# Kernel tuning notes

Measured on AMD Instinct MI355X. Metric: run time of the kernel, lower is better.

The kernel has to match this reference:

```python
import jax, jax.numpy as jnp
import numpy as np

N_NODES = 100000
N_EDGES = 1600000
IN_DIM, HIDDEN_DIM, OUT_DIM = 500, 64, 40


def setup_inputs() -> dict:
    key = jax.random.key(0)
    k1, k2, k3, k4, k5 = jax.random.split(key, 5)
    x = jax.random.normal(k1, (N_NODES, IN_DIM), dtype=jnp.float32)
    edge_index = jax.random.randint(k2, (2, N_EDGES), 0, N_NODES, dtype=jnp.int64)
    # Glorot-style init like PyG GCNConv
    W1 = jax.random.normal(k3, (IN_DIM, HIDDEN_DIM), dtype=jnp.float32) / np.sqrt(IN_DIM)
    b1 = jnp.zeros((HIDDEN_DIM,), dtype=jnp.float32)
    W2 = jax.random.normal(k4, (HIDDEN_DIM, OUT_DIM), dtype=jnp.float32) / np.sqrt(HIDDEN_DIM)
    b2 = jnp.zeros((OUT_DIM,), dtype=jnp.float32)
    return {"x": x, "W1": W1, "b1": b1, "W2": W2, "b2": b2, "edge_index": edge_index}


def _gcn_conv(x, W, b, src, dst, n):
    """PyG GCNConv: h = D^{-1/2} (A + I) D^{-1/2} (x W) + b."""
    h = x @ W  # transform first, propagate in smaller dim
    loops = jnp.arange(n, dtype=src.dtype)
    s = jnp.concatenate([src, loops])
    d = jnp.concatenate([dst, loops])
    deg = jax.ops.segment_sum(jnp.ones_like(d, dtype=h.dtype), d, num_segments=n)
    dinv = jnp.where(deg > 0, jax.lax.rsqrt(deg), 0.0)
    norm = dinv[s] * dinv[d]               # [E+N]
    msg = h[s] * norm[:, None]             # gather + scale
    out = jax.ops.segment_sum(msg, d, num_segments=n)  # scatter-add
    return out + b


def reference(x, W1, b1, W2, b2, edge_index):
    src, dst = edge_index[0], edge_index[1]
    n = x.shape[0]
    h = _gcn_conv(x, W1, b1, src, dst, n)
    h = jax.nn.relu(h)  # eval mode: dropout is identity
    out = _gcn_conv(h, W2, b2, src, dst, n)
    return out
```

## Files before the change

kernel.cpp:

```cpp
#include <hip/hip_runtime.h>
#include <cstdint>
#include <cstddef>

#define NN 100000
#define NE 1600000
#define IND 500
#define HD 64
#define OD 40
#define NBLK ((NN + 255) / 256)
#define KSTEPS 16
#define NTT 16
#define EB 1563

typedef __attribute__((ext_vector_type(8))) short short8v;
typedef __attribute__((ext_vector_type(8))) __bf16 bf16x8;
typedef __attribute__((ext_vector_type(4))) float float4v;

template <class V>
static __device__ __forceinline__ auto mfma_bf16_(V a, V b, float4v c, int)
    -> decltype(__builtin_amdgcn_mfma_f32_16x16x32_bf16(a, b, c, 0, 0, 0)) {
    return __builtin_amdgcn_mfma_f32_16x16x32_bf16(a, b, c, 0, 0, 0);
}
template <class V>
static __device__ __forceinline__ float4v mfma_bf16_(V a, V b, float4v c, long) {
    return __builtin_amdgcn_mfma_f32_16x16x32_bf16((bf16x8)a, (bf16x8)b, c, 0, 0, 0);
}
static __device__ __forceinline__ float4v mfma16(short8v a, short8v b, float4v c) {
    return mfma_bf16_(a, b, c, 0);
}

static __device__ __forceinline__ float bf2f(unsigned short v) {
    return __uint_as_float((unsigned)v << 16);
}
static __device__ __forceinline__ unsigned short f2bf(float v) {
    unsigned u = __float_as_uint(v);
    return (unsigned short)((u + 0x7fffu + ((u >> 16) & 1u)) >> 16);
}

typedef __attribute__((address_space(3))) char lds_char;
typedef const __attribute__((address_space(1))) char g_char;
static __device__ __forceinline__ void gl16(const char* g, char* l) {
    __builtin_amdgcn_global_load_lds((g_char*)g, (lds_char*)l, 16, 0, 0);
}

static __device__ __forceinline__ int detect64(const void* ei) {
    const unsigned* u = (const unsigned*)ei;
    int is64 = 1;
    #pragma unroll
    for (int i = 1; i < 16; i += 2)
        if (u[i] != 0u) is64 = 0;
    return is64;
}

static __device__ __forceinline__ void load4e(const void* ei, int is64, size_t base, int v[4]) {
    if (is64) {
        int4 a = ((const int4*)ei)[base >> 1];
        int4 b = ((const int4*)ei)[(base >> 1) + 1];
        v[0] = a.x; v[1] = a.z; v[2] = b.x; v[3] = b.z;
    } else {
        int4 a = *(const int4*)((const int*)ei + base);
        v[0] = a.x; v[1] = a.y; v[2] = a.z; v[3] = a.w;
    }
}

__global__ __launch_bounds__(256) void k_count_prep(const void* ei, int* cnt,
                                                    int* __restrict__ rank,
                                                    const float* __restrict__ W,
                                                    unsigned short* __restrict__ wh,
                                                    unsigned short* __restrict__ wl) {
    const int is64 = detect64(ei);
    int e0 = (blockIdx.x * 256 + threadIdx.x) * 4;
    if (e0 < NE) {
        int d[4];
        load4e(ei, is64, (size_t)NE + e0, d);
        int4 r;
        r.x = atomicAdd(&cnt[d[0]], 1);
        r.y = atomicAdd(&cnt[d[1]], 1);
        r.z = atomicAdd(&cnt[d[2]], 1);
        r.w = atomicAdd(&cnt[d[3]], 1);
        *(int4*)(rank + e0) = r;
    }
    int t = blockIdx.x * 256 + threadIdx.x;
    if (t < KSTEPS * 4 * 64) {
        int l = t & 63;
        int f = (t >> 6) & 3;
        int s = t >> 8;
        int n = f * 16 + (l & 15);
        int kbase = s * 32 + 8 * (l >> 4);
        unsigned short* ph = wh + (size_t)t * 8;
        unsigned short* pl = wl + (size_t)t * 8;
        #pragma unroll
        for (int j = 0; j < 8; ++j) {
            int k = kbase + j;
            float v = (k < IND) ? W[(size_t)k * HD + n] : 0.f;
            unsigned u = __float_as_uint(v);
            ph[j] = (unsigned short)(u >> 16);
            float r = v - __uint_as_float(u & 0xffff0000u);
            pl[j] = f2bf(r);
        }
    }
}

__global__ __launch_bounds__(256) void k_scan_block(const int* __restrict__ cnt,
                                                    int* __restrict__ rowptr,
                                                    int* __restrict__ bsum,
                                                    float* __restrict__ dinv) {
    int t = threadIdx.x;
    int i = blockIdx.x * 256 + t;
    int v = (i < NN) ? cnt[i] : 0;
    if (i < NN) dinv[i] = rsqrtf((float)v + 1.0f);
    int inc = v;
    #pragma unroll
    for (int off = 1; off < 64; off <<= 1) {
        int u = __shfl_up(inc, off);
        if ((t & 63) >= off) inc += u;
    }
    __shared__ int wsum[4];
    if ((t & 63) == 63) wsum[t >> 6] = inc;
    __syncthreads();
    if (t == 0) {
        int a = 0;
        #pragma unroll
        for (int w = 0; w < 4; ++w) { int b = wsum[w]; wsum[w] = a; a += b; }
        bsum[blockIdx.x] = a;
    }
    __syncthreads();
    if (i < NN) rowptr[i] = inc - v + wsum[t >> 6];
}

__global__ __launch_bounds__(512) void k_scan_bsum(int* bsum) {
    int t = threadIdx.x;
    int v = (t < NBLK) ? bsum[t] : 0;
    int inc = v;
    #pragma unroll
    for (int off = 1; off < 64; off <<= 1) {
        int u = __shfl_up(inc, off);
        if ((t & 63) >= off) inc += u;
    }
    __shared__ int wsum[8];
    if ((t & 63) == 63) wsum[t >> 6] = inc;
    __syncthreads();
    if (t == 0) {
        int a = 0;
        #pragma unroll
        for (int w = 0; w < 8; ++w) { int b = wsum[w]; wsum[w] = a; a += b; }
    }
    __syncthreads();
    if (t < NBLK) bsum[t] = inc - v + wsum[t >> 6];
}

__global__ void k_scan_add(int* rowptr, const int* __restrict__ bsum) {
    int i = blockIdx.x * 256 + threadIdx.x;
    if (i < NN) rowptr[i] += bsum[i >> 8];
    if (i == 0) rowptr[NN] = NE;
}

static __device__ __forceinline__ void split8f(float4 u0, float4 u1,
                                               short8v& hi, short8v& lo) {
    float t[8] = {u0.x, u0.y, u0.z, u0.w, u1.x, u1.y, u1.z, u1.w};
    #pragma unroll
    for (int j = 0; j < 8; ++j) {
        unsigned q = __float_as_uint(t[j]);
        hi[j] = (short)(q >> 16);
        float r = t[j] - __uint_as_float(q & 0xffff0000u);
        lo[j] = (short)f2bf(r);
    }
}

__global__ __launch_bounds__(256, 5) void k_gemm1m(const float* __restrict__ x,
                                                   const char* __restrict__ whb,
                                                   const char* __restrict__ wlb,
                                                   const float* __restrict__ dinv,
                                                   unsigned short* __restrict__ h,
                                                   const void* __restrict__ ei,
                                                   const int* __restrict__ rowptr,
                                                   const int* __restrict__ rank,
                                                   int* __restrict__ srcs) {
    __shared__ char smem[32768];
    const int tid  = threadIdx.x;
    const int lane = tid & 63;
    const int wave = tid >> 6;
    const int row0 = blockIdx.x * 64;
    const int rA = lane & 15;
    const int cg = lane >> 4;

    auto stage = [&](int kt, int buf) {
        const bool tail = (kt == NTT - 1);
        #pragma unroll
        for (int i = 0; i < 2; ++i) {
            int slot = i * 256 + tid;
            int r = slot >> 3, c = slot & 7;
            int cs = c ^ (r & 7);
            if (tail && cs > 4) cs = 4;
            int rsrc = row0 + r; if (rsrc >= NN) rsrc = NN - 1;
            const char* g = (const char*)x + (size_t)rsrc * (IND * 4) + kt * 128 + cs * 16;
            char* l = smem + buf * 16384 + (i * 256 + wave * 64) * 16;
            gl16(g, l);
        }
        #pragma unroll
        for (int i = 0; i < 2; ++i) {
            int j = i * 256 + tid;
            const char* src = (j < 256 ? whb : wlb) + kt * 4096 + (size_t)(j & 255) * 16;
            char* l = smem + buf * 16384 + 8192 + (i * 256 + wave * 64) * 16;
            gl16(src, l);
        }
    };

    float4v acc[4];
    const float4v zero4 = {0.f, 0.f, 0.f, 0.f};
    #pragma unroll
    for (int f = 0; f < 4; ++f) acc[f] = zero4;

    stage(0, 0);
    stage(1, 1);

    const int rbase = (wave * 16 + rA) * 8;
    const int sw = rA & 7;

    for (int kt = 0; kt < NTT; ++kt) {
        if (kt + 1 < NTT) asm volatile("s_waitcnt vmcnt(4)\ns_barrier" ::: "memory");
        else              asm volatile("s_waitcnt vmcnt(0)\ns_barrier" ::: "memory");
        const float4*  pa = (const float4*)(smem + (kt & 1) * 16384);
        const short8v* pb = (const short8v*)(smem + (kt & 1) * 16384 + 8192);
        int ch = cg * 2;
        float4 u0 = pa[rbase + (ch ^ sw)];
        float4 u1 = pa[rbase + ((ch + 1) ^ sw)];
        short8v ah, al;
        split8f(u0, u1, ah, al);
        #pragma unroll
        for (int f = 0; f < 4; ++f) {
            short8v vh = pb[f * 64 + lane];
            short8v vl = pb[256 + f * 64 + lane];
            acc[f] = mfma16(al, vh, acc[f]);
            acc[f] = mfma16(ah, vl, acc[f]);
            acc[f] = mfma16(ah, vh, acc[f]);
        }
        if (kt + 2 < NTT) {
            asm volatile("s_barrier" ::: "memory");
            stage(kt + 2, kt & 1);
        }
    }

    #pragma unroll
    for (int j = 0; j < 4; ++j) {
        int row = row0 + wave * 16 + cg * 4 + j;
        if (row < NN) {
            float dv = dinv[row];
            #pragma unroll
            for (int f = 0; f < 4; ++f)
                h[(size_t)row * HD + f * 16 + rA] = f2bf(acc[f][j] * dv);
        }
    }

    {
        int e0 = (blockIdx.x * 256 + tid) * 4;
        if (e0 < NE) {
            const int is64 = detect64(ei);
            int s[4], d[4];
            load4e(ei, is64, (size_t)e0, s);
            load4e(ei, is64, (size_t)NE + e0, d);
            int4 r = *(const int4*)(rank + e0);
            srcs[rowptr[d[0]] + r.x] = s[0];
            srcs[rowptr[d[1]] + r.y] = s[1];
            srcs[rowptr[d[2]] + r.z] = s[2];
            srcs[rowptr[d[3]] + r.w] = s[3];
        }
    }
}

static __device__ __forceinline__ float csr_gather(const int* __restrict__ rowptr,
                                                   const int* __restrict__ srcs,
                                                   const unsigned short* __restrict__ hb,
                                                   int wid, int lane, float acc) {
    int beg = rowptr[wid];
    int cnt = rowptr[wid + 1] - beg;
    for (int base = 0; base < cnt; base += 64) {
        int m = cnt - base; if (m > 64) m = 64;
        int sj = (lane < m) ? srcs[beg + base + lane] : 0;
        int j = 0;
        for (; j + 16 <= m; j += 16) {
            float v[16];
            #pragma unroll
            for (int q = 0; q < 16; ++q) {
                int sq = __builtin_amdgcn_readlane(sj, j + q);
                v[q] = bf2f(hb[(size_t)sq * HD + lane]);
            }
            float t0 = ((v[0] + v[1]) + (v[2] + v[3])) + ((v[4] + v[5]) + (v[6] + v[7]));
            float t1 = ((v[8] + v[9]) + (v[10] + v[11])) + ((v[12] + v[13]) + (v[14] + v[15]));
            acc += t0 + t1;
        }
        if (j + 8 <= m) {
            float v[8];
            #pragma unroll
            for (int q = 0; q < 8; ++q) {
                int sq = __builtin_amdgcn_readlane(sj, j + q);
                v[q] = bf2f(hb[(size_t)sq * HD + lane]);
            }
            acc += ((v[0] + v[1]) + (v[2] + v[3])) + ((v[4] + v[5]) + (v[6] + v[7]));
            j += 8;
        }
        for (; j < m; ++j) {
            int s = __builtin_amdgcn_readlane(sj, j);
            acc += bf2f(hb[(size_t)s * HD + lane]);
        }
    }
    return acc;
}

__global__ __launch_bounds__(256) void k_agg1(const int* __restrict__ rowptr,
                                              const int* __restrict__ srcs,
                                              const float* __restrict__ dinv,
                                              const unsigned short* __restrict__ hb,
                                              const float* __restrict__ bias,
                                              unsigned short* __restrict__ outb) {
    int wid = (blockIdx.x * 256 + threadIdx.x) >> 6;
    int lane = threadIdx.x & 63;
    if (wid >= NN) return;
    float acc = bf2f(hb[(size_t)wid * HD + lane]);
    acc = csr_gather(rowptr, srcs, hb, wid, lane, acc);
    float dn = dinv[wid];
    outb[(size_t)wid * HD + lane] = f2bf(fmaxf(acc * dn + bias[lane], 0.f) * dn);
}

__global__ __launch_bounds__(256) void k_agg2_gemm2(const int* __restrict__ rowptr,
                                                    const int* __restrict__ srcs,
                                                    const float* __restrict__ dinv,
                                                    const unsigned short* __restrict__ hb,
                                                    const float* __restrict__ W2,
                                                    const float* __restrict__ b2,
                                                    float* __restrict__ out) {
    __shared__ float ws2[HD][OD];
    __shared__ float hsh[4][HD];
    const int t = threadIdx.x;
    for (int i = t; i < HD * OD; i += 256)
        ws2[i / OD][i % OD] = W2[i];

    int wid = (blockIdx.x * 256 + t) >> 6;
    int lane = t & 63;
    int w = t >> 6;
    float acc = bf2f(hb[(size_t)wid * HD + lane]);
    acc = csr_gather(rowptr, srcs, hb, wid, lane, acc);
    hsh[w][lane] = acc * dinv[wid];
    __syncthreads();
    if (lane < OD) {
        float s = b2[lane];
        #pragma unroll
        for (int k = 0; k < HD; ++k)
            s = fmaf(hsh[w][k], ws2[k][lane], s);
        out[(size_t)wid * OD + lane] = s;
    }
}

extern "C" void kernel_launch(void* const* d_in, const int* in_sizes, int n_in,
                              void* d_out, int out_size, void* d_ws, size_t ws_size,
                              hipStream_t stream) {
    const float* x  = (const float*)d_in[0];
    const float* W1 = (const float*)d_in[1];
    const float* b1 = (const float*)d_in[2];
    const float* W2 = (const float*)d_in[3];
    const float* b2 = (const float*)d_in[4];
    const void*  ei = d_in[5];
    float* out = (float*)d_out;

    char* ws = (char*)d_ws;
    unsigned short* h1b    = (unsigned short*)ws;
    unsigned short* hrelub = (unsigned short*)(ws + 12800000);
    int*   rowptr = (int*)(ws + 25600000);
    int*   cnt    = (int*)(ws + 26000896);
    int*   bsum   = (int*)(ws + 26401792);
    int*   srcs   = (int*)(ws + 26403840);
    int*   rank   = (int*)(ws + 32803840);
    float* dinv   = (float*)(ws + 39203840);
    unsigned short* wh = (unsigned short*)(ws + 39604224);
    unsigned short* wl = (unsigned short*)(ws + 39669760);

    hipMemsetAsync(cnt, 0, (size_t)NN * 4, stream);
    k_count_prep<<<EB, 256, 0, stream>>>(ei, cnt, rank, W1, wh, wl);
    k_scan_block<<<NBLK, 256, 0, stream>>>(cnt, rowptr, bsum, dinv);
    k_scan_bsum<<<1, 512, 0, stream>>>(bsum);
    k_scan_add<<<NBLK, 256, 0, stream>>>(rowptr, bsum);
    k_gemm1m<<<EB, 256, 0, stream>>>(x, (const char*)wh, (const char*)wl, dinv, h1b,
                                     ei, rowptr, rank, srcs);
    k_agg1<<<(NN * 64) / 256, 256, 0, stream>>>(rowptr, srcs, dinv, h1b, b1, hrelub);
    k_agg2_gemm2<<<(NN * 64) / 256, 256, 0, stream>>>(rowptr, srcs, dinv, hrelub, W2, b2, out);
}
```

Baseline: 307.9 us.

## Enlarge GEMM1 tile to 128 rows and split CSR scatter into its own kernel

The first-layer GEMM now processes 128 rows per block, two 64-row M-subtiles, and reuses the loaded W1 hi/lo fragments across both subtiles. This halves the weight staging per row and the block count. The CSR source scatter, previously fused into the GEMM epilogue, moves to a separate kernel, and the memset is replaced by a zeroing kernel. The costs are higher LDS and register use (occupancy bound lowered from 5 to 3) and two extra kernel launches.

```diff
diff --git a/kernel.cpp b/kernel.cpp
--- a/kernel.cpp
+++ b/kernel.cpp
@@ -11,6 +11,7 @@
 #define KSTEPS 16
 #define NTT 16
 #define EB 1563
+#define GB 782
 
 typedef __attribute__((ext_vector_type(8))) short short8v;
 typedef __attribute__((ext_vector_type(8))) __bf16 bf16x8;
@@ -61,6 +62,11 @@
         int4 a = *(const int4*)((const int*)ei + base);
         v[0] = a.x; v[1] = a.y; v[2] = a.z; v[3] = a.w;
     }
+}
+
+__global__ void k_zero(int* __restrict__ cnt) {
+    int i = blockIdx.x * 256 + threadIdx.x;
+    if (i < NN) cnt[i] = 0;
 }
 
 __global__ __launch_bounds__(256) void k_count_prep(const void* ei, int* cnt,
@@ -155,6 +161,21 @@
     if (i == 0) rowptr[NN] = NE;
 }
 
+__global__ void k_scatter(const void* ei, const int* __restrict__ rowptr,
+                          const int* __restrict__ rank, int* __restrict__ srcs) {
+    int e0 = (blockIdx.x * 256 + threadIdx.x) * 4;
+    if (e0 >= NE) return;
+    const int is64 = detect64(ei);
+    int s[4], d[4];
+    load4e(ei, is64, (size_t)e0, s);
+    load4e(ei, is64, (size_t)NE + e0, d);
+    int4 r = *(const int4*)(rank + e0);
+    srcs[rowptr[d[0]] + r.x] = s[0];
+    srcs[rowptr[d[1]] + r.y] = s[1];
+    srcs[rowptr[d[2]] + r.z] = s[2];
+    srcs[rowptr[d[3]] + r.w] = s[3];
+}
+
 static __device__ __forceinline__ void split8f(float4 u0, float4 u1,
                                                short8v& hi, short8v& lo) {
     float t[8] = {u0.x, u0.y, u0.z, u0.w, u1.x, u1.y, u1.z, u1.w};
@@ -167,73 +188,78 @@
     }
 }
 
-__global__ __launch_bounds__(256, 5) void k_gemm1m(const float* __restrict__ x,
+__global__ __launch_bounds__(256, 3) void k_gemm1m(const float* __restrict__ x,
                                                    const char* __restrict__ whb,
                                                    const char* __restrict__ wlb,
                                                    const float* __restrict__ dinv,
-                                                   unsigned short* __restrict__ h,
-                                                   const void* __restrict__ ei,
-                                                   const int* __restrict__ rowptr,
-                                                   const int* __restrict__ rank,
-                                                   int* __restrict__ srcs) {
-    __shared__ char smem[32768];
+                                                   unsigned short* __restrict__ h) {
+    __shared__ char smem[49152];
     const int tid  = threadIdx.x;
     const int lane = tid & 63;
     const int wave = tid >> 6;
-    const int row0 = blockIdx.x * 64;
+    const int row0 = blockIdx.x * 128;
     const int rA = lane & 15;
     const int cg = lane >> 4;
 
     auto stage = [&](int kt, int buf) {
         const bool tail = (kt == NTT - 1);
         #pragma unroll
-        for (int i = 0; i < 2; ++i) {
+        for (int i = 0; i < 4; ++i) {
             int slot = i * 256 + tid;
             int r = slot >> 3, c = slot & 7;
             int cs = c ^ (r & 7);
             if (tail && cs > 4) cs = 4;
             int rsrc = row0 + r; if (rsrc >= NN) rsrc = NN - 1;
             const char* g = (const char*)x + (size_t)rsrc * (IND * 4) + kt * 128 + cs * 16;
-            char* l = smem + buf * 16384 + (i * 256 + wave * 64) * 16;
+            char* l = smem + buf * 24576 + (i * 256 + wave * 64) * 16;
             gl16(g, l);
         }
         #pragma unroll
         for (int i = 0; i < 2; ++i) {
             int j = i * 256 + tid;
             const char* src = (j < 256 ? whb : wlb) + kt * 4096 + (size_t)(j & 255) * 16;
-            char* l = smem + buf * 16384 + 8192 + (i * 256 + wave * 64) * 16;
+            char* l = smem + buf * 24576 + 16384 + (i * 256 + wave * 64) * 16;
             gl16(src, l);
         }
     };
 
-    float4v acc[4];
+    float4v acc[2][4];
     const float4v zero4 = {0.f, 0.f, 0.f, 0.f};
     #pragma unroll
-    for (int f = 0; f < 4; ++f) acc[f] = zero4;
+    for (int mi = 0; mi < 2; ++mi)
+        #pragma unroll
+        for (int f = 0; f < 4; ++f) acc[mi][f] = zero4;
 
     stage(0, 0);
     stage(1, 1);
 
-    const int rbase = (wave * 16 + rA) * 8;
     const int sw = rA & 7;
+    const int ch = cg * 2;
 
     for (int kt = 0; kt < NTT; ++kt) {
-        if (kt + 1 < NTT) asm volatile("s_waitcnt vmcnt(4)\ns_barrier" ::: "memory");
+        if (kt + 1 < NTT) asm volatile("s_waitcnt vmcnt(6)\ns_barrier" ::: "memory");
         else              asm volatile("s_waitcnt vmcnt(0)\ns_barrier" ::: "memory");
-        const float4*  pa = (const float4*)(smem + (kt & 1) * 16384);
-        const short8v* pb = (const short8v*)(smem + (kt & 1) * 16384 + 8192);
-        int ch = cg * 2;
-        float4 u0 = pa[rbase + (ch ^ sw)];
-        float4 u1 = pa[rbase + ((ch + 1) ^ sw)];
-        short8v ah, al;
-        split8f(u0, u1, ah, al);
+        const float4*  pa = (const float4*)(smem + (kt & 1) * 24576);
+        const short8v* pb = (const short8v*)(smem + (kt & 1) * 24576 + 16384);
+        short8v vh[4], vl[4];
         #pragma unroll
         for (int f = 0; f < 4; ++f) {
-            short8v vh = pb[f * 64 + lane];
-            short8v vl = pb[256 + f * 64 + lane];
-            acc[f] = mfma16(al, vh, acc[f]);
-            acc[f] = mfma16(ah, vl, acc[f]);
-            acc[f] = mfma16(ah, vh, acc[f]);
+            vh[f] = pb[f * 64 + lane];
+            vl[f] = pb[256 + f * 64 + lane];
+        }
+        #pragma unroll
+        for (int mi = 0; mi < 2; ++mi) {
+            int rb = (mi * 64 + wave * 16 + rA) * 8;
+            float4 u0 = pa[rb + (ch ^ sw)];
+            float4 u1 = pa[rb + ((ch + 1) ^ sw)];
+            short8v ah, al;
+            split8f(u0, u1, ah, al);
+            #pragma unroll
+            for (int f = 0; f < 4; ++f) {
+                acc[mi][f] = mfma16(al, vh[f], acc[mi][f]);
+                acc[mi][f] = mfma16(ah, vl[f], acc[mi][f]);
+                acc[mi][f] = mfma16(ah, vh[f], acc[mi][f]);
+            }
         }
         if (kt + 2 < NTT) {
             asm volatile("s_barrier" ::: "memory");
@@ -242,30 +268,17 @@
     }
 
     #pragma unroll
-    for (int j = 0; j < 4; ++j) {
-        int row = row0 + wave * 16 + cg * 4 + j;
-        if (row < NN) {
-            float dv = dinv[row];
-            #pragma unroll
-            for (int f = 0; f < 4; ++f)
-                h[(size_t)row * HD + f * 16 + rA] = f2bf(acc[f][j] * dv);
-        }
-    }
-
-    {
-        int e0 = (blockIdx.x * 256 + tid) * 4;
-        if (e0 < NE) {
-            const int is64 = detect64(ei);
-            int s[4], d[4];
-            load4e(ei, is64, (size_t)e0, s);
-            load4e(ei, is64, (size_t)NE + e0, d);
-            int4 r = *(const int4*)(rank + e0);
-            srcs[rowptr[d[0]] + r.x] = s[0];
-            srcs[rowptr[d[1]] + r.y] = s[1];
-            srcs[rowptr[d[2]] + r.z] = s[2];
-            srcs[rowptr[d[3]] + r.w] = s[3];
-        }
-    }
+    for (int mi = 0; mi < 2; ++mi)
+        #pragma unroll
+        for (int j = 0; j < 4; ++j) {
+            int row = row0 + mi * 64 + wave * 16 + cg * 4 + j;
+            if (row < NN) {
+                float dv = dinv[row];
+                #pragma unroll
+                for (int f = 0; f < 4; ++f)
+                    h[(size_t)row * HD + f * 16 + rA] = f2bf(acc[mi][f][j] * dv);
+            }
+        }
 }
 
 static __device__ __forceinline__ float csr_gather(const int* __restrict__ rowptr,
@@ -374,13 +387,13 @@
     unsigned short* wh = (unsigned short*)(ws + 39604224);
     unsigned short* wl = (unsigned short*)(ws + 39669760);
 
-    hipMemsetAsync(cnt, 0, (size_t)NN * 4, stream);
+    k_zero<<<NBLK, 256, 0, stream>>>(cnt);
     k_count_prep<<<EB, 256, 0, stream>>>(ei, cnt, rank, W1, wh, wl);
     k_scan_block<<<NBLK, 256, 0, stream>>>(cnt, rowptr, bsum, dinv);
     k_scan_bsum<<<1, 512, 0, stream>>>(bsum);
     k_scan_add<<<NBLK, 256, 0, stream>>>(rowptr, bsum);
-    k_gemm1m<<<EB, 256, 0, stream>>>(x, (const char*)wh, (const char*)wl, dinv, h1b,
-                                     ei, rowptr, rank, srcs);
+    k_scatter<<<EB, 256, 0, stream>>>(ei, rowptr, rank, srcs);
+    k_gemm1m<<<GB, 256, 0, stream>>>(x, (const char*)wh, (const char*)wl, dinv, h1b);
     k_agg1<<<(NN * 64) / 256, 256, 0, stream>>>(rowptr, srcs, dinv, h1b, b1, hrelub);
     k_agg2_gemm2<<<(NN * 64) / 256, 256, 0, stream>>>(rowptr, srcs, dinv, hrelub, W2, b2, out);
 }
```

New measurement: 320.8 us. 4.2% more time.

## Vectorize CSR gather to 4 edges per wave and split scatter kernel

Applied to the files above, without the earlier changes.

The CSR aggregation now has each wave handle four neighbour rows at once. Each group of 16 lanes loads 8 bytes (four bf16 features) per neighbour instead of one 2-byte element per lane, and partial sums are folded across lane groups with xor shuffles. The aim is wider, fewer memory transactions for the random-row gathers in both aggregation kernels. Separately, the edge-to-CSR scatter moves out of the GEMM kernel into its own launch, which adds a kernel launch but removes the scatter tail from the GEMM blocks. Sums are now accumulated in a different order, so results may differ slightly in rounding.

```diff
diff --git a/kernel.cpp b/kernel.cpp
--- a/kernel.cpp
+++ b/kernel.cpp
@@ -155,6 +155,21 @@
     if (i == 0) rowptr[NN] = NE;
 }
 
+__global__ void k_scatter(const void* ei, const int* __restrict__ rowptr,
+                          const int* __restrict__ rank, int* __restrict__ srcs) {
+    int e0 = (blockIdx.x * 256 + threadIdx.x) * 4;
+    if (e0 >= NE) return;
+    const int is64 = detect64(ei);
+    int s[4], d[4];
+    load4e(ei, is64, (size_t)e0, s);
+    load4e(ei, is64, (size_t)NE + e0, d);
+    int4 r = *(const int4*)(rank + e0);
+    srcs[rowptr[d[0]] + r.x] = s[0];
+    srcs[rowptr[d[1]] + r.y] = s[1];
+    srcs[rowptr[d[2]] + r.z] = s[2];
+    srcs[rowptr[d[3]] + r.w] = s[3];
+}
+
 static __device__ __forceinline__ void split8f(float4 u0, float4 u1,
                                                short8v& hi, short8v& lo) {
     float t[8] = {u0.x, u0.y, u0.z, u0.w, u1.x, u1.y, u1.z, u1.w};
@@ -171,11 +186,7 @@
                                                    const char* __restrict__ whb,
                                                    const char* __restrict__ wlb,
                                                    const float* __restrict__ dinv,
-                                                   unsigned short* __restrict__ h,
-                                                   const void* __restrict__ ei,
-                                                   const int* __restrict__ rowptr,
-                                                   const int* __restrict__ rank,
-                                                   int* __restrict__ srcs) {
+                                                   unsigned short* __restrict__ h) {
     __shared__ char smem[32768];
     const int tid  = threadIdx.x;
     const int lane = tid & 63;
@@ -251,27 +262,14 @@
                 h[(size_t)row * HD + f * 16 + rA] = f2bf(acc[f][j] * dv);
         }
     }
-
-    {
-        int e0 = (blockIdx.x * 256 + tid) * 4;
-        if (e0 < NE) {
-            const int is64 = detect64(ei);
-            int s[4], d[4];
-            load4e(ei, is64, (size_t)e0, s);
-            load4e(ei, is64, (size_t)NE + e0, d);
-            int4 r = *(const int4*)(rank + e0);
-            srcs[rowptr[d[0]] + r.x] = s[0];
-            srcs[rowptr[d[1]] + r.y] = s[1];
-            srcs[rowptr[d[2]] + r.z] = s[2];
-            srcs[rowptr[d[3]] + r.w] = s[3];
-        }
-    }
-}
-
-static __device__ __forceinline__ float csr_gather(const int* __restrict__ rowptr,
+}
+
+static __device__ __forceinline__ void csr_gather4(const int* __restrict__ rowptr,
                                                    const int* __restrict__ srcs,
                                                    const unsigned short* __restrict__ hb,
-                                                   int wid, int lane, float acc) {
+                                                   int wid, int lane, float acc4[4]) {
+    const int c4 = lane & 15;
+    const int ng = lane >> 4;
     int beg = rowptr[wid];
     int cnt = rowptr[wid + 1] - beg;
     for (int base = 0; base < cnt; base += 64) {
@@ -279,32 +277,42 @@
         int sj = (lane < m) ? srcs[beg + base + lane] : 0;
         int j = 0;
         for (; j + 16 <= m; j += 16) {
-            float v[16];
+            int si[4];
             #pragma unroll
-            for (int q = 0; q < 16; ++q) {
-                int sq = __builtin_amdgcn_readlane(sj, j + q);
-                v[q] = bf2f(hb[(size_t)sq * HD + lane]);
+            for (int q = 0; q < 4; ++q)
+                si[q] = __shfl(sj, j + q * 4 + ng);
+            uint2 v[4];
+            #pragma unroll
+            for (int q = 0; q < 4; ++q)
+                v[q] = *(const uint2*)(hb + (size_t)si[q] * HD + c4 * 4);
+            #pragma unroll
+            for (int q = 0; q < 4; ++q) {
+                acc4[0] += bf2f((unsigned short)(v[q].x & 0xffffu));
+                acc4[1] += bf2f((unsigned short)(v[q].x >> 16));
+                acc4[2] += bf2f((unsigned short)(v[q].y & 0xffffu));
+                acc4[3] += bf2f((unsigned short)(v[q].y >> 16));
             }
-            float t0 = ((v[0] + v[1]) + (v[2] + v[3])) + ((v[4] + v[5]) + (v[6] + v[7]));
-            float t1 = ((v[8] + v[9]) + (v[10] + v[11])) + ((v[12] + v[13]) + (v[14] + v[15]));
-            acc += t0 + t1;
-        }
-        if (j + 8 <= m) {
-            float v[8];
-            #pragma unroll
-            for (int q = 0; q < 8; ++q) {
-                int sq = __builtin_amdgcn_readlane(sj, j + q);
-                v[q] = bf2f(hb[(size_t)sq * HD + lane]);
+        }
+        for (; j < m; j += 4) {
+            int idx = j + ng;
+            int s = __shfl(sj, idx < m ? idx : j);
+            if (idx < m) {
+                uint2 v = *(const uint2*)(hb + (size_t)s * HD + c4 * 4);
+                acc4[0] += bf2f((unsigned short)(v.x & 0xffffu));
+                acc4[1] += bf2f((unsigned short)(v.x >> 16));
+                acc4[2] += bf2f((unsigned short)(v.y & 0xffffu));
+                acc4[3] += bf2f((unsigned short)(v.y >> 16));
             }
-            acc += ((v[0] + v[1]) + (v[2] + v[3])) + ((v[4] + v[5]) + (v[6] + v[7]));
-            j += 8;
-        }
-        for (; j < m; ++j) {
-            int s = __builtin_amdgcn_readlane(sj, j);
-            acc += bf2f(hb[(size_t)s * HD + lane]);
-        }
-    }
-    return acc;
+        }
+    }
+}
+
+static __device__ __forceinline__ void fold4(float acc4[4]) {
+    #pragma unroll
+    for (int k = 0; k < 4; ++k) {
+        acc4[k] += __shfl_xor(acc4[k], 16);
+        acc4[k] += __shfl_xor(acc4[k], 32);
+    }
 }
 
 __global__ __launch_bounds__(256) void k_agg1(const int* __restrict__ rowptr,
@@ -316,10 +324,27 @@
     int wid = (blockIdx.x * 256 + threadIdx.x) >> 6;
     int lane = threadIdx.x & 63;
     if (wid >= NN) return;
-    float acc = bf2f(hb[(size_t)wid * HD + lane]);
-    acc = csr_gather(rowptr, srcs, hb, wid, lane, acc);
-    float dn = dinv[wid];
-    outb[(size_t)wid * HD + lane] = f2bf(fmaxf(acc * dn + bias[lane], 0.f) * dn);
+    const int c4 = lane & 15;
+    const int ng = lane >> 4;
+    float acc4[4] = {0.f, 0.f, 0.f, 0.f};
+    if (ng == 0) {
+        uint2 v = *(const uint2*)(hb + (size_t)wid * HD + c4 * 4);
+        acc4[0] = bf2f((unsigned short)(v.x & 0xffffu));
+        acc4[1] = bf2f((unsigned short)(v.x >> 16));
+        acc4[2] = bf2f((unsigned short)(v.y & 0xffffu));
+        acc4[3] = bf2f((unsigned short)(v.y >> 16));
+    }
+    csr_gather4(rowptr, srcs, hb, wid, lane, acc4);
+    fold4(acc4);
+    if (ng == 0) {
+        float dn = dinv[wid];
+        float4 bv = *(const float4*)(bias + c4 * 4);
+        unsigned r0 = (unsigned)f2bf(fmaxf(acc4[0] * dn + bv.x, 0.f) * dn)
+                    | ((unsigned)f2bf(fmaxf(acc4[1] * dn + bv.y, 0.f) * dn) << 16);
+        unsigned r1 = (unsigned)f2bf(fmaxf(acc4[2] * dn + bv.z, 0.f) * dn)
+                    | ((unsigned)f2bf(fmaxf(acc4[3] * dn + bv.w, 0.f) * dn) << 16);
+        *(uint2*)(outb + (size_t)wid * HD + c4 * 4) = make_uint2(r0, r1);
+    }
 }
 
 __global__ __launch_bounds__(256) void k_agg2_gemm2(const int* __restrict__ rowptr,
@@ -338,9 +363,25 @@
     int wid = (blockIdx.x * 256 + t) >> 6;
     int lane = t & 63;
     int w = t >> 6;
-    float acc = bf2f(hb[(size_t)wid * HD + lane]);
-    acc = csr_gather(rowptr, srcs, hb, wid, lane, acc);
-    hsh[w][lane] = acc * dinv[wid];
+    const int c4 = lane & 15;
+    const int ng = lane >> 4;
+    float acc4[4] = {0.f, 0.f, 0.f, 0.f};
+    if (ng == 0) {
+        uint2 v = *(const uint2*)(hb + (size_t)wid * HD + c4 * 4);
+        acc4[0] = bf2f((unsigned short)(v.x & 0xffffu));
+        acc4[1] = bf2f((unsigned short)(v.x >> 16));
+        acc4[2] = bf2f((unsigned short)(v.y & 0xffffu));
+        acc4[3] = bf2f((unsigned short)(v.y >> 16));
+    }
+    csr_gather4(rowptr, srcs, hb, wid, lane, acc4);
+    fold4(acc4);
+    if (ng == 0) {
+        float dn = dinv[wid];
+        hsh[w][c4 * 4 + 0] = acc4[0] * dn;
+        hsh[w][c4 * 4 + 1] = acc4[1] * dn;
+        hsh[w][c4 * 4 + 2] = acc4[2] * dn;
+        hsh[w][c4 * 4 + 3] = acc4[3] * dn;
+    }
     __syncthreads();
     if (lane < OD) {
         float s = b2[lane];
@@ -379,8 +420,8 @@
     k_scan_block<<<NBLK, 256, 0, stream>>>(cnt, rowptr, bsum, dinv);
     k_scan_bsum<<<1, 512, 0, stream>>>(bsum);
     k_scan_add<<<NBLK, 256, 0, stream>>>(rowptr, bsum);
-    k_gemm1m<<<EB, 256, 0, stream>>>(x, (const char*)wh, (const char*)wl, dinv, h1b,
-                                     ei, rowptr, rank, srcs);
+    k_scatter<<<EB, 256, 0, stream>>>(ei, rowptr, rank, srcs);
+    k_gemm1m<<<EB, 256, 0, stream>>>(x, (const char*)wh, (const char*)wl, dinv, h1b);
     k_agg1<<<(NN * 64) / 256, 256, 0, stream>>>(rowptr, srcs, dinv, h1b, b1, hrelub);
     k_agg2_gemm2<<<(NN * 64) / 256, 256, 0, stream>>>(rowptr, srcs, dinv, hrelub, W2, b2, out);
 }
```

New measurement: 308.3 us. About the same (+0.1%).
